# Kernel tuning notes

Measured on AMD Instinct MI355X. Metric: run time of the kernel, lower is better.

The kernel has to match this reference:

```python
import jax, jax.numpy as jnp
import numpy as np

N = 100000
E = 1600000
K = 15        # kernel_size (num Gaussian mixture components)
DIM = 3       # pseudo-coordinate dim
EPS = 1e-15   # PyG GMMConv sigma epsilon
BN_EPS = 1e-5
CH = [(50, 75), (75, 100), (100, 75), (75, 50)]


def setup_inputs() -> dict:
    key = jax.random.key(0)
    ks = iter(jax.random.split(key, 64))
    inp = {}
    inp["x"] = jax.random.normal(next(ks), (N, 50), jnp.float32)
    inp["edge_index"] = jax.random.randint(next(ks), (2, E), 0, N, jnp.int64)
    inp["edge_attr"] = jax.random.uniform(next(ks), (E, DIM), jnp.float32)
    for l, (cin, cout) in enumerate(CH, 1):
        inp[f"g{l}"] = jax.random.normal(next(ks), (cin, K, cout), jnp.float32) * 0.1
        inp[f"mu{l}"] = jax.random.normal(next(ks), (K, DIM), jnp.float32)
        inp[f"sigma{l}"] = jnp.ones((K, DIM), jnp.float32) + 0.1 * jax.random.uniform(next(ks), (K, DIM), jnp.float32)
        inp[f"root{l}"] = jax.random.normal(next(ks), (cin, cout), jnp.float32) * 0.1
        inp[f"b{l}"] = jax.random.normal(next(ks), (cout,), jnp.float32) * 0.01
        if l < 4:
            inp[f"gamma{l}"] = jnp.ones((cout,), jnp.float32)
            inp[f"beta{l}"] = jnp.zeros((cout,), jnp.float32)
    return inp


def gmm_layer(x, src, tgt, pseudo, g, mu, sigma, root, bias):
    # Gaussian mixture edge weights: w[e,k] = exp(-0.5 * sum_d (u_ed - mu_kd)^2 / sigma_kd^2)
    n = x.shape[0]
    diff = pseudo[:, None, :] - mu[None, :, :]              # [E,K,dim]
    w = jnp.exp(-0.5 * jnp.sum(diff * diff / (sigma[None] ** 2 + EPS), axis=-1))  # [E,K]
    xs = x[src]                                             # gather source feats [E,Cin]
    # out_t = sum_k (sum_{e->t} w_ek * x_src[e]) @ G_k  (avoids [E,K,Cout] tensor)
    agg = jnp.zeros((n, g.shape[2]), x.dtype)
    for k in range(K):
        zk = jax.ops.segment_sum(xs * w[:, k:k + 1], tgt, num_segments=n)  # [N,Cin]
        agg = agg + zk @ g[:, k, :]
    deg = jax.ops.segment_sum(jnp.ones((src.shape[0],), x.dtype), tgt, num_segments=n)
    agg = agg / jnp.maximum(deg, 1.0)[:, None]              # aggr='mean'
    return agg + x @ root + bias


def batchnorm(x, gamma, beta):
    m = jnp.mean(x, axis=0)
    v = jnp.var(x, axis=0)
    return gamma * (x - m) * jax.lax.rsqrt(v + BN_EPS) + beta


def reference(x, edge_index, edge_attr,
              g1, mu1, sigma1, root1, b1, gamma1, beta1,
              g2, mu2, sigma2, root2, b2, gamma2, beta2,
              g3, mu3, sigma3, root3, b3, gamma3, beta3,
              g4, mu4, sigma4, root4, b4):
    src, tgt = edge_index[0], edge_index[1]
    h = jax.nn.elu(gmm_layer(x, src, tgt, edge_attr, g1, mu1, sigma1, root1, b1))
    h = batchnorm(h, gamma1, beta1)
    h = jax.nn.elu(gmm_layer(h, src, tgt, edge_attr, g2, mu2, sigma2, root2, b2))
    h = batchnorm(h, gamma2, beta2)
    h = jax.nn.elu(gmm_layer(h, src, tgt, edge_attr, g3, mu3, sigma3, root3, b3))
    h = batchnorm(h, gamma3, beta3)
    return gmm_layer(h, src, tgt, edge_attr, g4, mu4, sigma4, root4, b4)
```

## Files before the change

kernel.cpp:

```cpp
#include <hip/hip_runtime.h>
#include <stdint.h>

#define NN 100000
#define NE 1600000
#define KG 15

typedef unsigned short u16;
typedef __attribute__((ext_vector_type(8))) short short8;
typedef __attribute__((ext_vector_type(8))) __bf16 bf16x8;
typedef __attribute__((ext_vector_type(4))) float f32x4;

static __device__ __forceinline__ float bf2f(u16 u){ return __uint_as_float(((unsigned)u)<<16); }
static __device__ __forceinline__ u16 f2bf(float f){
  unsigned u = __float_as_uint(f);
  u += 0x7FFFu + ((u>>16)&1u);
  return (u16)(u>>16);
}
static __device__ __forceinline__ float ldf(const void* p, long long i, int isf32){
  return isf32 ? ((const float*)p)[i] : bf2f(((const u16*)p)[i]);
}
static __device__ __forceinline__ int ld_idx(const void* p, long long i, int isi64){
  return isi64 ? (int)((const long long*)p)[i] : ((const int*)p)[i];
}
static __device__ __forceinline__ f32x4 mfma16x16x32(short8 a, short8 b, f32x4 c){
  return __builtin_amdgcn_mfma_f32_16x16x32_bf16(
      __builtin_bit_cast(bf16x8, a), __builtin_bit_cast(bf16x8, b), c, 0, 0, 0);
}

__global__ void k_sentinel(float* out, float val){
  if (threadIdx.x == 0 && blockIdx.x == 0) out[0] = val;
}

__global__ void k_probe(const void* sg1, const void* ei, int* flags){
  if (threadIdx.x == 0 && blockIdx.x == 0){
    const u16* p = (const u16*)sg1;
    int sane = 1;
    for (int i=0;i<45;i++){ float v = bf2f(p[i]); if (!(v > 0.5f && v < 2.0f)) sane = 0; }
    flags[0] = sane ? 0 : 1;
    const int* q = (const int*)ei;
    int allz = 1;
    for (int i=1;i<128;i+=2) if (q[i] != 0) allz = 0;
    flags[1] = allz ? 1 : 0;
  }
}

__global__ __launch_bounds__(256) void k_convx(const void* x, u16* xcv, const int* flags){
  int i = blockIdx.x*256 + threadIdx.x;
  int c = i & 63, r = i >> 6;
  if (r >= NN) return;
  int isf = flags[0];
  u16 v = 0;
  if (c < 50){
    long long s = (long long)r*50 + c;
    v = isf ? f2bf(((const float*)x)[s]) : ((const u16*)x)[s];
  }
  xcv[(size_t)r*64 + c] = v;
}

__global__ __launch_bounds__(256) void k_deg(const void* ei, int* __restrict__ deg, const int* flags){
  int e = blockIdx.x*256 + threadIdx.x;
  int isi64 = flags[1];
  atomicAdd(&deg[ld_idx(ei, (long long)NE + e, isi64)], 1);
}

__global__ __launch_bounds__(256) void k_scan1(const int* __restrict__ deg, int* __restrict__ rp,
                                               int* __restrict__ bsum){
  __shared__ int lds[256];
  int b = blockIdx.x, t = threadIdx.x;
  int base = b*1024 + t*4;
  int v[4]; int s = 0;
  #pragma unroll
  for (int i=0;i<4;i++){ v[i] = (base+i < NN) ? deg[base+i] : 0; s += v[i]; }
  lds[t] = s; __syncthreads();
  int inc = s;
  for (int off=1; off<256; off<<=1){
    int y = (t>=off) ? lds[t-off] : 0;
    __syncthreads();
    inc += y; lds[t] = inc;
    __syncthreads();
  }
  int excl = inc - s;
  #pragma unroll
  for (int i=0;i<4;i++){ if (base+i < NN) rp[base+i] = excl; excl += v[i]; }
  if (t == 255) bsum[b] = inc;
}

__global__ __launch_bounds__(128) void k_scan2(int* __restrict__ bsum, int* __restrict__ rp){
  __shared__ int lds[128];
  int t = threadIdx.x;
  const int nb = (NN + 1023)/1024;
  int s = (t < nb) ? bsum[t] : 0;
  lds[t] = s; __syncthreads();
  int inc = s;
  for (int off=1; off<128; off<<=1){
    int y = (t>=off) ? lds[t-off] : 0;
    __syncthreads();
    inc += y; lds[t] = inc;
    __syncthreads();
  }
  bsum[t] = inc - s;
  if (t == 0) rp[NN] = NE;
}

__global__ __launch_bounds__(256) void k_scan3(int* __restrict__ rp, const int* __restrict__ bsum){
  int b = blockIdx.x, t = threadIdx.x;
  int add = bsum[b];
  int base = b*1024 + t*4;
  #pragma unroll
  for (int i=0;i<4;i++) if (base+i < NN) rp[base+i] += add;
}

__global__ __launch_bounds__(256) void k_fill(const void* ei, const void* attr,
                                              const int* __restrict__ rp, int* __restrict__ cur,
                                              int* __restrict__ perm, int4* __restrict__ csr16,
                                              int emode, const int* flags){
  int e = blockIdx.x*256 + threadIdx.x;
  int isf = flags[0], isi64 = flags[1];
  int t = ld_idx(ei, (long long)NE + e, isi64);
  int p = rp[t] + atomicAdd(&cur[t], 1);
  if (emode){
    int s = ld_idx(ei, e, isi64);
    float u0 = ldf(attr, 3LL*e+0, isf), u1 = ldf(attr, 3LL*e+1, isf), u2 = ldf(attr, 3LL*e+2, isf);
    csr16[p] = make_int4(s, __float_as_int(u0), __float_as_int(u1), __float_as_int(u2));
  } else {
    perm[p] = e;
  }
}

__global__ __launch_bounds__(256) void k_repack(const void* g, const void* root,
                                                u16* __restrict__ bp, int KC, int CIN, int COUT,
                                                int KS, int NCT, const int* flags){
  int tid = blockIdx.x*256 + threadIdx.x;
  int total = NCT*KS*64;
  if (tid >= total) return;
  int isf = flags[0];
  int lane = tid & 63;
  int ks = (tid >> 6) % KS;
  int ct = tid / (64*KS);
  int c = ct*16 + (lane & 15);
  int kbase = ks*32 + (lane >> 4)*8;
  short8 v8 = {};
  #pragma unroll
  for (int j=0;j<8;j++){
    int kk = kbase + j; u16 v = 0;
    if (c < COUT){
      if (kk < KC){
        int k = kk / CIN, cin = kk - k*CIN;
        v = f2bf(ldf(g, ((long long)cin*KG + k)*COUT + c, isf));
      } else if (kk < KC + CIN){
        v = f2bf(ldf(root, (long long)(kk-KC)*COUT + c, isf));
      }
    }
    v8[j] = (short)v;
  }
  ((short8*)bp)[tid] = v8;
}

template<int CIN, int COUT, int KPAD, int NCT, int XS, bool EM16, bool FINAL>
__global__ __launch_bounds__(512) void k_fused(
    const int4* __restrict__ csr16, const int* __restrict__ perm,
    const void* ei, const void* attr, const int* __restrict__ rp,
    const u16* __restrict__ xin, const void* mu, const void* sg,
    const u16* __restrict__ bp, const void* bias,
    u16* __restrict__ h, float* __restrict__ outp, const int* flags)
{
  constexpr int KC   = CIN*KG;
  constexpr int NT   = (CIN + 15)/16;
  constexpr int RS   = KPAD + 8;
  constexpr int KS   = KPAD/32;
  __shared__ short8 zsh[16*RS/8];
  u16* zb = (u16*)zsh;

  int isf = flags[0], isi64 = flags[1];
  int wv = threadIdx.x >> 6, lane = threadIdx.x & 63;
  int m = lane & 15, q = lane >> 4;
  int node0 = blockIdx.x * 16;

  bool kvalid = (m < KG);
  int mm = kvalid ? m : 0;
  float mu0 = ldf(mu, mm*3+0, isf), mu1 = ldf(mu, mm*3+1, isf), mu2 = ldf(mu, mm*3+2, isf);
  float s0 = ldf(sg, mm*3+0, isf),  s1 = ldf(sg, mm*3+1, isf),  s2 = ldf(sg, mm*3+2, isf);
  float is0 = 1.f/(s0*s0 + 1e-15f), is1 = 1.f/(s1*s1 + 1e-15f), is2 = 1.f/(s2*s2 + 1e-15f);

  #pragma unroll 1
  for (int s = 0; s < 2; s++){
    int r = wv*2 + s;
    int t = node0 + r;
    int rs = rp[t], re = rp[t+1];
    f32x4 acc[NT] = {};
    int lastE = re - 1;
    for (int base = rs; base < re; base += 32){
      int e0 = base + q*8;
      float u0[8], u1[8], u2[8];
      int srcs[8];
      if (EM16){
        int4 ce[8];
        #pragma unroll
        for (int j=0;j<8;j++){
          int ep = e0 + j; ep = (ep > lastE) ? lastE : ep;
          ce[j] = csr16[ep];
        }
        #pragma unroll
        for (int j=0;j<8;j++){
          srcs[j] = ce[j].x;
          u0[j] = __int_as_float(ce[j].y); u1[j] = __int_as_float(ce[j].z); u2[j] = __int_as_float(ce[j].w);
        }
      } else {
        int eix[8];
        #pragma unroll
        for (int j=0;j<8;j++){
          int ep = e0 + j; ep = (ep > lastE) ? lastE : ep;
          eix[j] = perm[ep];
        }
        #pragma unroll
        for (int j=0;j<8;j++) srcs[j] = ld_idx(ei, eix[j], isi64);
        #pragma unroll
        for (int j=0;j<8;j++){
          u0[j] = ldf(attr, 3LL*eix[j]+0, isf);
          u1[j] = ldf(attr, 3LL*eix[j]+1, isf);
          u2[j] = ldf(attr, 3LL*eix[j]+2, isf);
        }
      }
      short8 af;
      #pragma unroll
      for (int j=0;j<8;j++){
        float d0 = u0[j] - mu0, d1 = u1[j] - mu1, d2 = u2[j] - mu2;
        float w = __expf(-0.5f*(d0*d0*is0 + d1*d1*is1 + d2*d2*is2));
        bool ok = kvalid && (e0 + j <= lastE);
        w = ok ? w : 0.f;
        af[j] = (short)f2bf(w);
      }
      #pragma unroll
      for (int ct=0; ct<NT; ct++){
        int cin = ct*16 + m;
        int cc = (cin < CIN) ? cin : (CIN-1);
        u16 xv[8];
        #pragma unroll
        for (int j=0;j<8;j++) xv[j] = xin[(size_t)srcs[j]*XS + cc];
        short8 bf;
        #pragma unroll
        for (int j=0;j<8;j++) bf[j] = (cin < CIN) ? (short)xv[j] : (short)0;
        acc[ct] = mfma16x16x32(af, bf, acc[ct]);
      }
    }

    int dg = re - rs;
    float inv = 1.f / (float)(dg > 0 ? dg : 1);
    u16* row = zb + r*RS;
    #pragma unroll
    for (int ct=0; ct<NT; ct++){
      int cin = ct*16 + m;
      if (cin < CIN){
        #pragma unroll
        for (int rr=0;rr<4;rr++){
          int k = q*4 + rr;
          if (k < KG) row[k*CIN + cin] = f2bf(acc[ct][rr]*inv);
        }
      }
    }
    for (int idx = lane; idx < KPAD - KC; idx += 64){
      u16 v = 0;
      if (idx < CIN) v = xin[(size_t)t*XS + idx];
      row[KC + idx] = v;
    }
  }

  __syncthreads();

  if (wv < NCT){
    const short8* bpv = (const short8*)bp;
    const short8* zv  = (const short8*)zsh;
    f32x4 a0 = {}, a1 = {};
    #pragma unroll 2
    for (int ks=0; ks+1<KS; ks+=2){
      short8 af0 = zv[m*(RS/8) + ks*4 + q];
      short8 bf0 = bpv[(wv*KS + ks)*64 + lane];
      a0 = mfma16x16x32(af0, bf0, a0);
      short8 af1 = zv[m*(RS/8) + (ks+1)*4 + q];
      short8 bf1 = bpv[(wv*KS + ks+1)*64 + lane];
      a1 = mfma16x16x32(af1, bf1, a1);
    }
    if (KS & 1){
      short8 af0 = zv[m*(RS/8) + (KS-1)*4 + q];
      short8 bf0 = bpv[(wv*KS + KS-1)*64 + lane];
      a0 = mfma16x16x32(af0, bf0, a0);
    }
    f32x4 acc = a0 + a1;
    int col = wv*16 + m;
    if (col < COUT){
      float bv = ldf(bias, col, isf);
      #pragma unroll
      for (int rr=0;rr<4;rr++){
        int rrow = node0 + q*4 + rr;
        float v = acc[rr] + bv;
        if (!FINAL){
          v = (v > 0.f) ? v : (__expf(v) - 1.f);
          h[(size_t)rrow*COUT + col] = f2bf(v);
        } else {
          outp[(size_t)rrow*COUT + col] = v;
        }
      }
    }
  }
}

__global__ __launch_bounds__(256) void k_stats(const u16* __restrict__ h, float* __restrict__ sums,
                                               float* __restrict__ sumsq, int COUT){
  __shared__ float sS[256], sQ[256];
  int t = threadIdx.x;
  int c = t & 127, rg = t >> 7;
  float s = 0.f, qq = 0.f;
  int r0 = blockIdx.x*512 + rg*256;
  if (c < COUT){
    for (int i=0;i<256;i++){
      int r = r0 + i;
      if (r < NN){ float v = bf2f(h[(size_t)r*COUT + c]); s += v; qq += v*v; }
    }
  }
  sS[t] = s; sQ[t] = qq; __syncthreads();
  if (t < 128){
    float a = sS[t] + sS[t+128];
    float b = sQ[t] + sQ[t+128];
    if (t < COUT){ atomicAdd(&sums[t], a); atomicAdd(&sumsq[t], b); }
  }
}

__global__ __launch_bounds__(256) void k_bn(const u16* __restrict__ h, const void* gamma,
                                            const void* beta, const float* __restrict__ sums,
                                            const float* __restrict__ sumsq, u16* __restrict__ xo,
                                            int COUT, const int* flags){
  int t = threadIdx.x;
  int isf = flags[0];
  int c = t & 127;
  int r = blockIdx.x*2 + (t >> 7);
  if (r >= NN) return;
  if (c >= COUT){
    if (c < 128) xo[(size_t)r*128 + c] = 0;
    return;
  }
  const float invn = 1.f/(float)NN;
  float mean = sums[c]*invn;
  float var  = sumsq[c]*invn - mean*mean;
  float g = ldf(gamma, c, isf), b = ldf(beta, c, isf);
  float v = g*(bf2f(h[(size_t)r*COUT + c]) - mean)*rsqrtf(var + 1e-5f) + b;
  xo[(size_t)r*128 + c] = f2bf(v);
}

extern "C" void kernel_launch(void* const* d_in, const int* in_sizes, int n_in,
                              void* d_out, int out_size, void* d_ws, size_t ws_size,
                              hipStream_t stream)
{
  static const int expected[29] = {
    5000000, 3200000, 4800000,
    56250, 45, 45, 3750, 75, 75, 75,
    112500, 45, 45, 7500, 100, 100, 100,
    112500, 45, 45, 7500, 75, 75, 75,
    56250, 45, 45, 3750, 50
  };
  if (n_in != 29){ k_sentinel<<<1, 64, 0, stream>>>((float*)d_out, 512.0f); return; }
  for (int j=0;j<29;j++){
    if (in_sizes[j] != expected[j]){
      k_sentinel<<<1, 64, 0, stream>>>((float*)d_out, 1024.0f*(float)(1+j));
      return;
    }
  }

  const void* x0   = d_in[0];
  const void* ei   = d_in[1];
  const void* attr = d_in[2];
  const void* G[4]  = {d_in[3],  d_in[10], d_in[17], d_in[24]};
  const void* MU[4] = {d_in[4],  d_in[11], d_in[18], d_in[25]};
  const void* SG[4] = {d_in[5],  d_in[12], d_in[19], d_in[26]};
  const void* RT[4] = {d_in[6],  d_in[13], d_in[20], d_in[27]};
  const void* BI[4] = {d_in[7],  d_in[14], d_in[21], d_in[28]};
  const void* GA[3] = {d_in[8],  d_in[15], d_in[22]};
  const void* BE[3] = {d_in[9],  d_in[16], d_in[23]};

  char* w = (char*)d_ws;
  auto alloc = [&](size_t bytes)->char*{ char* p = w; w += (bytes + 255) & ~(size_t)255; return p; };
  int*  flags = (int*) alloc(256);
  int*  deg  = (int*) alloc((size_t)NN*4);
  int*  cur  = (int*) alloc((size_t)NN*4);
  int*  rp   = (int*) alloc((size_t)(NN+1)*4);
  int*  bsum = (int*) alloc(512*4);
  u16*  h    = (u16*) alloc((size_t)NN*100*2);
  u16*  xb   = (u16*) alloc((size_t)NN*128*2);
  u16*  bp   = (u16*) alloc(1<<19);
  float* sums  = (float*)alloc(512);
  float* sumsq = (float*)alloc(512);
  u16*  xcv  = xb + (size_t)NN*64;

  size_t base = (size_t)(w - (char*)d_ws);
  int emode; int* perm = nullptr; int4* csr16 = nullptr;
  if (ws_size >= base + (size_t)NE*16 + 4096){
    emode = 1; csr16 = (int4*)alloc((size_t)NE*16);
  } else if (ws_size >= base + (size_t)NE*4 + 4096){
    emode = 0; perm = (int*)alloc((size_t)NE*4);
  } else {
    float mb = (float)(ws_size >> 20); if (mb > 255.f) mb = 255.f;
    k_sentinel<<<1, 64, 0, stream>>>((float*)d_out, 65536.0f + 256.0f*mb);
    return;
  }

  k_probe<<<1, 64, 0, stream>>>(SG[0], ei, flags);
  k_convx<<<NN*64/256, 256, 0, stream>>>(x0, xcv, flags);

  hipMemsetAsync(deg, 0, (size_t)NN*4, stream);
  hipMemsetAsync(cur, 0, (size_t)NN*4, stream);
  k_deg  <<<NE/256, 256, 0, stream>>>(ei, deg, flags);
  k_scan1<<<(NN+1023)/1024, 256, 0, stream>>>(deg, rp, bsum);
  k_scan2<<<1, 128, 0, stream>>>(bsum, rp);
  k_scan3<<<(NN+1023)/1024, 256, 0, stream>>>(rp, bsum);
  k_fill <<<NE/256, 256, 0, stream>>>(ei, attr, rp, cur, perm, csr16, emode, flags);

  const int NB = NN/16;

  {
    k_repack<<<(5*25*64 + 255)/256, 256, 0, stream>>>(G[0], RT[0], bp, 750, 50, 75, 25, 5, flags);
    if (emode) k_fused<50,75,800,5,64,true ,false><<<NB,512,0,stream>>>(csr16, perm, ei, attr, rp, xcv, MU[0], SG[0], bp, BI[0], h, nullptr, flags);
    else       k_fused<50,75,800,5,64,false,false><<<NB,512,0,stream>>>(csr16, perm, ei, attr, rp, xcv, MU[0], SG[0], bp, BI[0], h, nullptr, flags);
    hipMemsetAsync(sums, 0, 512, stream); hipMemsetAsync(sumsq, 0, 512, stream);
    k_stats<<<(NN+511)/512, 256, 0, stream>>>(h, sums, sumsq, 75);
    k_bn<<<NN/2, 256, 0, stream>>>(h, GA[0], BE[0], sums, sumsq, xb, 75, flags);
  }

  {
    k_repack<<<(7*38*64 + 255)/256, 256, 0, stream>>>(G[1], RT[1], bp, 1125, 75, 100, 38, 7, flags);
    if (emode) k_fused<75,100,1216,7,128,true ,false><<<NB,512,0,stream>>>(csr16, perm, ei, attr, rp, xb, MU[1], SG[1], bp, BI[1], h, nullptr, flags);
    else       k_fused<75,100,1216,7,128,false,false><<<NB,512,0,stream>>>(csr16, perm, ei, attr, rp, xb, MU[1], SG[1], bp, BI[1], h, nullptr, flags);
    hipMemsetAsync(sums, 0, 512, stream); hipMemsetAsync(sumsq, 0, 512, stream);
    k_stats<<<(NN+511)/512, 256, 0, stream>>>(h, sums, sumsq, 100);
    k_bn<<<NN/2, 256, 0, stream>>>(h, GA[1], BE[1], sums, sumsq, xb, 100, flags);
  }

  {
    k_repack<<<(5*50*64 + 255)/256, 256, 0, stream>>>(G[2], RT[2], bp, 1500, 100, 75, 50, 5, flags);
    if (emode) k_fused<100,75,1600,5,128,true ,false><<<NB,512,0,stream>>>(csr16, perm, ei, attr, rp, xb, MU[2], SG[2], bp, BI[2], h, nullptr, flags);
    else       k_fused<100,75,1600,5,128,false,false><<<NB,512,0,stream>>>(csr16, perm, ei, attr, rp, xb, MU[2], SG[2], bp, BI[2], h, nullptr, flags);
    hipMemsetAsync(sums, 0, 512, stream); hipMemsetAsync(sumsq, 0, 512, stream);
    k_stats<<<(NN+511)/512, 256, 0, stream>>>(h, sums, sumsq, 75);
    k_bn<<<NN/2, 256, 0, stream>>>(h, GA[2], BE[2], sums, sumsq, xb, 75, flags);
  }

  {
    k_repack<<<(4*38*64 + 255)/256, 256, 0, stream>>>(G[3], RT[3], bp, 1125, 75, 50, 38, 4, flags);
    if (emode) k_fused<75,50,1216,4,128,true ,true><<<NB,512,0,stream>>>(csr16, perm, ei, attr, rp, xb, MU[3], SG[3], bp, BI[3], nullptr, (float*)d_out, flags);
    else       k_fused<75,50,1216,4,128,false,true><<<NB,512,0,stream>>>(csr16, perm, ei, attr, rp, xb, MU[3], SG[3], bp, BI[3], nullptr, (float*)d_out, flags);
  }
}
```

Before: 1.276 ms.

## Fuse batchnorm statistics into GMM kernel and gather paired channels per load

Per-column sum and sum-of-squares for batchnorm are now reduced inside the fused layer kernel epilogue with shuffles and atomics, which removes the separate k_stats pass that re-read h. The edge gather now loads two adjacent bf16 channels per 32-bit access and splits them into even and odd MFMA operands, which halves the number of gather loads per edge. The channel mapping of the accumulators changes to match. In exchange there are many more atomics (one per 16-node block per column) and slightly more register pressure.

```diff
diff --git a/kernel.cpp b/kernel.cpp
--- a/kernel.cpp
+++ b/kernel.cpp
@@ -162,10 +162,12 @@
     const void* ei, const void* attr, const int* __restrict__ rp,
     const u16* __restrict__ xin, const void* mu, const void* sg,
     const u16* __restrict__ bp, const void* bias,
-    u16* __restrict__ h, float* __restrict__ outp, const int* flags)
+    u16* __restrict__ h, float* __restrict__ outp,
+    float* __restrict__ sums, float* __restrict__ sumsq, const int* flags)
 {
   constexpr int KC   = CIN*KG;
-  constexpr int NT   = (CIN + 15)/16;
+  constexpr int P    = (CIN + 31)/32;
+  constexpr int NA   = 2*P;
   constexpr int RS   = KPAD + 8;
   constexpr int KS   = KPAD/32;
   __shared__ short8 zsh[16*RS/8];
@@ -187,7 +189,7 @@
     int r = wv*2 + s;
     int t = node0 + r;
     int rs = rp[t], re = rp[t+1];
-    f32x4 acc[NT] = {};
+    f32x4 acc[NA] = {};
     int lastE = re - 1;
     for (int base = rs; base < re; base += 32){
       int e0 = base + q*8;
@@ -231,16 +233,21 @@
         af[j] = (short)f2bf(w);
       }
       #pragma unroll
-      for (int ct=0; ct<NT; ct++){
-        int cin = ct*16 + m;
-        int cc = (cin < CIN) ? cin : (CIN-1);
-        u16 xv[8];
-        #pragma unroll
-        for (int j=0;j<8;j++) xv[j] = xin[(size_t)srcs[j]*XS + cc];
-        short8 bf;
-        #pragma unroll
-        for (int j=0;j<8;j++) bf[j] = (cin < CIN) ? (short)xv[j] : (short)0;
-        acc[ct] = mfma16x16x32(af, bf, acc[ct]);
+      for (int p=0; p<P; p++){
+        unsigned xw[8];
+        #pragma unroll
+        for (int j=0;j<8;j++)
+          xw[j] = *(const unsigned*)(xin + (size_t)srcs[j]*XS + p*32 + 2*m);
+        int cin_e = p*32 + 2*m;
+        bool ve = (cin_e < CIN), vo = (cin_e + 1 < CIN);
+        short8 bfe, bfo;
+        #pragma unroll
+        for (int j=0;j<8;j++){
+          bfe[j] = ve ? (short)(xw[j] & 0xffffu) : (short)0;
+          bfo[j] = vo ? (short)(xw[j] >> 16) : (short)0;
+        }
+        acc[2*p]   = mfma16x16x32(af, bfe, acc[2*p]);
+        acc[2*p+1] = mfma16x16x32(af, bfo, acc[2*p+1]);
       }
     }
 
@@ -248,8 +255,8 @@
     float inv = 1.f / (float)(dg > 0 ? dg : 1);
     u16* row = zb + r*RS;
     #pragma unroll
-    for (int ct=0; ct<NT; ct++){
-      int cin = ct*16 + m;
+    for (int ct=0; ct<NA; ct++){
+      int cin = (ct>>1)*32 + 2*m + (ct&1);
       if (cin < CIN){
         #pragma unroll
         for (int rr=0;rr<4;rr++){
@@ -289,39 +296,30 @@
     int col = wv*16 + m;
     if (col < COUT){
       float bv = ldf(bias, col, isf);
+      float vs[4];
       #pragma unroll
       for (int rr=0;rr<4;rr++){
         int rrow = node0 + q*4 + rr;
         float v = acc[rr] + bv;
         if (!FINAL){
           v = (v > 0.f) ? v : (__expf(v) - 1.f);
+          vs[rr] = v;
           h[(size_t)rrow*COUT + col] = f2bf(v);
         } else {
           outp[(size_t)rrow*COUT + col] = v;
         }
       }
-    }
-  }
-}
-
-__global__ __launch_bounds__(256) void k_stats(const u16* __restrict__ h, float* __restrict__ sums,
-                                               float* __restrict__ sumsq, int COUT){
-  __shared__ float sS[256], sQ[256];
-  int t = threadIdx.x;
-  int c = t & 127, rg = t >> 7;
-  float s = 0.f, qq = 0.f;
-  int r0 = blockIdx.x*512 + rg*256;
-  if (c < COUT){
-    for (int i=0;i<256;i++){
-      int r = r0 + i;
-      if (r < NN){ float v = bf2f(h[(size_t)r*COUT + c]); s += v; qq += v*v; }
-    }
-  }
-  sS[t] = s; sQ[t] = qq; __syncthreads();
-  if (t < 128){
-    float a = sS[t] + sS[t+128];
-    float b = sQ[t] + sQ[t+128];
-    if (t < COUT){ atomicAdd(&sums[t], a); atomicAdd(&sumsq[t], b); }
+      if (!FINAL){
+        float ss = vs[0]+vs[1]+vs[2]+vs[3];
+        float qq = vs[0]*vs[0]+vs[1]*vs[1]+vs[2]*vs[2]+vs[3]*vs[3];
+        ss += __shfl_xor(ss, 16); ss += __shfl_xor(ss, 32);
+        qq += __shfl_xor(qq, 16); qq += __shfl_xor(qq, 32);
+        if (q == 0){
+          atomicAdd(&sums[col], ss);
+          atomicAdd(&sumsq[col], qq);
+        }
+      }
+    }
   }
 }
 
@@ -417,34 +415,31 @@
 
   {
     k_repack<<<(5*25*64 + 255)/256, 256, 0, stream>>>(G[0], RT[0], bp, 750, 50, 75, 25, 5, flags);
-    if (emode) k_fused<50,75,800,5,64,true ,false><<<NB,512,0,stream>>>(csr16, perm, ei, attr, rp, xcv, MU[0], SG[0], bp, BI[0], h, nullptr, flags);
-    else       k_fused<50,75,800,5,64,false,false><<<NB,512,0,stream>>>(csr16, perm, ei, attr, rp, xcv, MU[0], SG[0], bp, BI[0], h, nullptr, flags);
     hipMemsetAsync(sums, 0, 512, stream); hipMemsetAsync(sumsq, 0, 512, stream);
-    k_stats<<<(NN+511)/512, 256, 0, stream>>>(h, sums, sumsq, 75);
+    if (emode) k_fused<50,75,800,5,64,true ,false><<<NB,512,0,stream>>>(csr16, perm, ei, attr, rp, xcv, MU[0], SG[0], bp, BI[0], h, nullptr, sums, sumsq, flags);
+    else       k_fused<50,75,800,5,64,false,false><<<NB,512,0,stream>>>(csr16, perm, ei, attr, rp, xcv, MU[0], SG[0], bp, BI[0], h, nullptr, sums, sumsq, flags);
     k_bn<<<NN/2, 256, 0, stream>>>(h, GA[0], BE[0], sums, sumsq, xb, 75, flags);
   }
 
   {
     k_repack<<<(7*38*64 + 255)/256, 256, 0, stream>>>(G[1], RT[1], bp, 1125, 75, 100, 38, 7, flags);
-    if (emode) k_fused<75,100,1216,7,128,true ,false><<<NB,512,0,stream>>>(csr16, perm, ei, attr, rp, xb, MU[1], SG[1], bp, BI[1], h, nullptr, flags);
-    else       k_fused<75,100,1216,7,128,false,false><<<NB,512,0,stream>>>(csr16, perm, ei, attr, rp, xb, MU[1], SG[1], bp, BI[1], h, nullptr, flags);
     hipMemsetAsync(sums, 0, 512, stream); hipMemsetAsync(sumsq, 0, 512, stream);
-    k_stats<<<(NN+511)/512, 256, 0, stream>>>(h, sums, sumsq, 100);
+    if (emode) k_fused<75,100,1216,7,128,true ,false><<<NB,512,0,stream>>>(csr16, perm, ei, attr, rp, xb, MU[1], SG[1], bp, BI[1], h, nullptr, sums, sumsq, flags);
+    else       k_fused<75,100,1216,7,128,false,false><<<NB,512,0,stream>>>(csr16, perm, ei, attr, rp, xb, MU[1], SG[1], bp, BI[1], h, nullptr, sums, sumsq, flags);
     k_bn<<<NN/2, 256, 0, stream>>>(h, GA[1], BE[1], sums, sumsq, xb, 100, flags);
   }
 
   {
     k_repack<<<(5*50*64 + 255)/256, 256, 0, stream>>>(G[2], RT[2], bp, 1500, 100, 75, 50, 5, flags);
-    if (emode) k_fused<100,75,1600,5,128,true ,false><<<NB,512,0,stream>>>(csr16, perm, ei, attr, rp, xb, MU[2], SG[2], bp, BI[2], h, nullptr, flags);
-    else       k_fused<100,75,1600,5,128,false,false><<<NB,512,0,stream>>>(csr16, perm, ei, attr, rp, xb, MU[2], SG[2], bp, BI[2], h, nullptr, flags);
     hipMemsetAsync(sums, 0, 512, stream); hipMemsetAsync(sumsq, 0, 512, stream);
-    k_stats<<<(NN+511)/512, 256, 0, stream>>>(h, sums, sumsq, 75);
+    if (emode) k_fused<100,75,1600,5,128,true ,false><<<NB,512,0,stream>>>(csr16, perm, ei, attr, rp, xb, MU[2], SG[2], bp, BI[2], h, nullptr, sums, sumsq, flags);
+    else       k_fused<100,75,1600,5,128,false,false><<<NB,512,0,stream>>>(csr16, perm, ei, attr, rp, xb, MU[2], SG[2], bp, BI[2], h, nullptr, sums, sumsq, flags);
     k_bn<<<NN/2, 256, 0, stream>>>(h, GA[2], BE[2], sums, sumsq, xb, 75, flags);
   }
 
   {
     k_repack<<<(4*38*64 + 255)/256, 256, 0, stream>>>(G[3], RT[3], bp, 1125, 75, 50, 38, 4, flags);
-    if (emode) k_fused<75,50,1216,4,128,true ,true><<<NB,512,0,stream>>>(csr16, perm, ei, attr, rp, xb, MU[3], SG[3], bp, BI[3], nullptr, (float*)d_out, flags);
-    else       k_fused<75,50,1216,4,128,false,true><<<NB,512,0,stream>>>(csr16, perm, ei, attr, rp, xb, MU[3], SG[3], bp, BI[3], nullptr, (float*)d_out, flags);
-  }
-}
+    if (emode) k_fused<75,50,1216,4,128,true ,true><<<NB,512,0,stream>>>(csr16, perm, ei, attr, rp, xb, MU[3], SG[3], bp, BI[3], nullptr, (float*)d_out, sums, sumsq, flags);
+    else       k_fused<75,50,1216,4,128,false,true><<<NB,512,0,stream>>>(csr16, perm, ei, attr, rp, xb, MU[3], SG[3], bp, BI[3], nullptr, (float*)d_out, sums, sumsq, flags);
+  }
+}
```

Result: faster. 1.116 ms (-12.6%).
